# Optimization experiments

Hardware: AMD Instinct MI355X
Metric: run time of the kernel (lower is better)

Reference implementation:

```python
import jax, jax.numpy as jnp
import numpy as np
import math

EPS = 1e-5
GROUPS = 8


def setup_inputs() -> dict:
    key = jax.random.key(0)
    ks = jax.random.split(key, 4)
    B, C, H, W = 16, 256, 32, 32
    x = jax.random.normal(ks[0], (B, C, H, W), dtype=jnp.float32)
    gamma = jnp.ones((C,), dtype=jnp.float32)
    beta = jnp.zeros((C,), dtype=jnp.float32)
    # 1x1 convs are per-pixel matmuls; store weights as [out, in]
    w_qkv = jax.random.normal(ks[1], (3 * C, C), dtype=jnp.float32) * (1.0 / math.sqrt(C))
    b_qkv = jnp.zeros((3 * C,), dtype=jnp.float32)
    w_proj = jax.random.normal(ks[2], (C, C), dtype=jnp.float32) * (1.0 / math.sqrt(C))
    b_proj = jnp.zeros((C,), dtype=jnp.float32)
    return {"x": x, "gamma": gamma, "beta": beta, "w_qkv": w_qkv,
            "b_qkv": b_qkv, "w_proj": w_proj, "b_proj": b_proj}


def group_norm(x, gamma, beta):
    B, C, H, W = x.shape
    xg = x.reshape(B, GROUPS, (C // GROUPS) * H * W)
    mean = jnp.mean(xg, axis=-1, keepdims=True)
    var = jnp.var(xg, axis=-1, keepdims=True)
    xn = ((xg - mean) * jax.lax.rsqrt(var + EPS)).reshape(B, C, H, W)
    return xn * gamma[None, :, None, None] + beta[None, :, None, None]


def reference(x, gamma, beta, w_qkv, b_qkv, w_proj, b_proj):
    B, C, H, W = x.shape
    N = H * W
    residual = x
    xn = group_norm(x, gamma, beta)
    # 1x1 conv QKV: [B,3C,H,W]
    qkv = jnp.einsum('bchw,oc->bohw', xn, w_qkv) + b_qkv[None, :, None, None]
    q, k, v = jnp.split(qkv, 3, axis=1)
    q = q.reshape(B, C, N).transpose(0, 2, 1)   # [B,N,C]
    k = k.reshape(B, C, N)                      # [B,C,N]
    v = v.reshape(B, C, N).transpose(0, 2, 1)   # [B,N,C]
    attn = jnp.einsum('bnc,bcm->bnm', q, k) / math.sqrt(C)
    attn = jax.nn.softmax(attn, axis=-1)
    out = jnp.einsum('bnm,bmc->bnc', attn, v)   # [B,N,C]
    out = out.transpose(0, 2, 1).reshape(B, C, H, W)
    out = jnp.einsum('bchw,oc->bohw', out, w_proj) + b_proj[None, :, None, None]
    return out + residual
```

## Files before the change

kernel.cpp:

```cpp
#include <hip/hip_runtime.h>

typedef __bf16 bf16_t;
typedef __bf16 bf16x8 __attribute__((ext_vector_type(8)));
typedef float f32x4 __attribute__((ext_vector_type(4)));
typedef unsigned short u16;
typedef unsigned int u32;

#define MFMA16(a, b, c) __builtin_amdgcn_mfma_f32_16x16x32_bf16((a), (b), (c), 0, 0, 0)

__device__ __forceinline__ void gld_lds16(const bf16_t* g, bf16_t* l) {
  __builtin_amdgcn_global_load_lds(
      (const __attribute__((address_space(1))) void*)g,
      (__attribute__((address_space(3))) void*)l, 16, 0, 0);
}

__device__ inline bool is_f32_flag(const void* gamma) {
  return *(const u32*)gamma == 0x3F800000u;
}

template <typename T>
__device__ inline void load8f(const T* p, float* d) {
  if constexpr (sizeof(T) == 2) {
    bf16x8 v = *(const bf16x8*)p;
#pragma unroll
    for (int j = 0; j < 8; ++j) d[j] = (float)v[j];
  } else {
    float4 a = *(const float4*)p;
    float4 b = *(const float4*)(p + 4);
    d[0] = a.x; d[1] = a.y; d[2] = a.z; d[3] = a.w;
    d[4] = b.x; d[5] = b.y; d[6] = b.z; d[7] = b.w;
  }
}

__device__ inline void store8bf(bf16_t* dst, const float* s) {
  bf16x8 v;
#pragma unroll
  for (int j = 0; j < 8; ++j) v[j] = (bf16_t)s[j];
  *(bf16x8*)dst = v;
}

template <typename T>
__device__ void gn_body(const T* __restrict__ x, const T* __restrict__ gamma,
                        const T* __restrict__ beta, bf16_t* __restrict__ xn_t,
                        float* red, float* gm, float* bt) {
  const int g = blockIdx.x, b = blockIdx.y, tid = threadIdx.x;
  const T* xg = x + ((size_t)b * 256 + g * 32) * 1024;
  float sum = 0.f, sq = 0.f, v8[8];
  for (int i = tid * 8; i < 32768; i += 2048) {
    load8f(xg + i, v8);
#pragma unroll
    for (int j = 0; j < 8; ++j) { sum += v8[j]; sq += v8[j] * v8[j]; }
  }
#pragma unroll
  for (int off = 32; off; off >>= 1) {
    sum += __shfl_xor(sum, off);
    sq  += __shfl_xor(sq, off);
  }
  const int w = tid >> 6;
  if ((tid & 63) == 0) { red[w * 2] = sum; red[w * 2 + 1] = sq; }
  __syncthreads();
  sum = red[0] + red[2] + red[4] + red[6];
  sq  = red[1] + red[3] + red[5] + red[7];
  const float mean = sum * (1.f / 32768.f);
  const float var  = sq * (1.f / 32768.f) - mean * mean;
  const float rstd = rsqrtf(var + 1e-5f);
  if (tid < 32) {
    gm[tid] = (float)gamma[g * 32 + tid] * rstd;
    bt[tid] = (float)beta[g * 32 + tid];
  }
  __syncthreads();
  for (int q = 0; q < 4; ++q) {
    const int n = q * 256 + tid;
    bf16_t* dst = xn_t + ((size_t)b * 1024 + n) * 256 + g * 32;
#pragma unroll
    for (int c8 = 0; c8 < 4; ++c8) {
      bf16x8 o;
#pragma unroll
      for (int j = 0; j < 8; ++j) {
        const int c = c8 * 8 + j;
        o[j] = (bf16_t)(((float)xg[(size_t)c * 1024 + n] - mean) * gm[c] + bt[c]);
      }
      *(bf16x8*)(dst + c8 * 8) = o;
    }
  }
}

__global__ __launch_bounds__(256) void gn_kernel(const void* x, const void* gamma,
                                                 const void* beta, bf16_t* xn_t) {
  __shared__ float red[8];
  __shared__ float gm[32], bt[32];
  if (is_f32_flag(gamma))
    gn_body<float>((const float*)x, (const float*)gamma, (const float*)beta, xn_t, red, gm, bt);
  else
    gn_body<bf16_t>((const bf16_t*)x, (const bf16_t*)gamma, (const bf16_t*)beta, xn_t, red, gm, bt);
}

template <int MODE, typename T>
__device__ void gemm_body(const T* __restrict__ A, const bf16_t* __restrict__ Bt,
                          const T* __restrict__ bias, const T* __restrict__ xres,
                          void* O0v, bf16_t* __restrict__ O1, bf16_t* __restrict__ O2,
                          bf16_t* sA, bf16_t* sB) {
  const int tid = threadIdx.x;
  const int n0 = blockIdx.x * 128, m0 = blockIdx.y * 128, b = blockIdx.z;
  const bf16_t* Bb = Bt + (size_t)b * (1024 * 256);
  const int w = tid >> 6, lane = tid & 63, ln = lane & 15, quad = lane >> 4;
  const int wm = w >> 1, wn = w & 1;
  f32x4 acc[4][4] = {};
  const int sr = tid >> 3, sc = (tid & 7) * 8;
  for (int kb = 0; kb < 4; ++kb) {
    const int k0 = kb * 64;
    float t[8];
#pragma unroll 4
    for (int rr = sr; rr < 128; rr += 32) {
      load8f(A + (size_t)(m0 + rr) * 256 + k0 + sc, t);
      store8bf(sA + rr * 72 + sc, t);
      *(uint4*)(sB + rr * 72 + sc) = *(const uint4*)(Bb + (size_t)(n0 + rr) * 256 + k0 + sc);
    }
    __syncthreads();
#pragma unroll
    for (int ks = 0; ks < 2; ++ks) {
      bf16x8 af[4], bfr[4];
#pragma unroll
      for (int mt = 0; mt < 4; ++mt)
        af[mt] = *(const bf16x8*)(sA + (wm * 64 + mt * 16 + ln) * 72 + ks * 32 + quad * 8);
#pragma unroll
      for (int nt = 0; nt < 4; ++nt)
        bfr[nt] = *(const bf16x8*)(sB + (wn * 64 + nt * 16 + ln) * 72 + ks * 32 + quad * 8);
#pragma unroll
      for (int mt = 0; mt < 4; ++mt)
#pragma unroll
        for (int nt = 0; nt < 4; ++nt)
          acc[mt][nt] = MFMA16(af[mt], bfr[nt], acc[mt][nt]);
    }
    __syncthreads();
  }
  if (MODE == 0) {
    if (m0 < 512) {
      const float scale = (m0 < 256) ? 0.0625f * 1.44269504f : 1.0f;
      bf16_t* dstBase = ((m0 < 256) ? (bf16_t*)O0v : O1) + (size_t)b * (1024 * 256);
      const int osub = (m0 < 256) ? 0 : 256;
#pragma unroll
      for (int mt = 0; mt < 4; ++mt) {
        const int ob = m0 + wm * 64 + mt * 16 + quad * 4;
        float bi[4];
#pragma unroll
        for (int r = 0; r < 4; ++r) bi[r] = (float)bias[ob + r];
#pragma unroll
        for (int nt = 0; nt < 4; ++nt) {
          const int n = n0 + wn * 64 + nt * 16 + ln;
          ushort4 pk;
#pragma unroll
          for (int r = 0; r < 4; ++r) {
            bf16_t h = (bf16_t)((acc[mt][nt][r] + bi[r]) * scale);
            ((u16*)&pk)[r] = __builtin_bit_cast(u16, h);
          }
          *(ushort4*)(dstBase + (size_t)n * 256 + (ob - osub)) = pk;
        }
      }
    } else {
      bf16_t* dstV = O2 + (size_t)b * (256 * 1024);
#pragma unroll
      for (int mt = 0; mt < 4; ++mt) {
        const int ob = m0 + wm * 64 + mt * 16 + quad * 4;
        float bi[4];
#pragma unroll
        for (int r = 0; r < 4; ++r) bi[r] = (float)bias[ob + r];
#pragma unroll
        for (int nt = 0; nt < 4; ++nt) {
          const int n = n0 + wn * 64 + nt * 16 + ln;
#pragma unroll
          for (int r = 0; r < 4; ++r)
            dstV[(size_t)(ob + r - 512) * 1024 + n] = (bf16_t)(acc[mt][nt][r] + bi[r]);
        }
      }
    }
  } else {
    T* O0 = (T*)O0v;
#pragma unroll
    for (int mt = 0; mt < 4; ++mt) {
      const int ob = m0 + wm * 64 + mt * 16 + quad * 4;
      float bi[4];
#pragma unroll
      for (int r = 0; r < 4; ++r) bi[r] = (float)bias[ob + r];
#pragma unroll
      for (int nt = 0; nt < 4; ++nt) {
        const int n = n0 + wn * 64 + nt * 16 + ln;
#pragma unroll
        for (int r = 0; r < 4; ++r) {
          const size_t idx = ((size_t)b * 256 + ob + r) * 1024 + n;
          O0[idx] = (T)(acc[mt][nt][r] + bi[r] + (float)xres[idx]);
        }
      }
    }
  }
}

template <int MODE>
__global__ __launch_bounds__(256) void gemm_bt_kernel(
    const void* gflag, const void* A, const bf16_t* Bt, const void* bias,
    const void* xres, void* O0, bf16_t* O1, bf16_t* O2) {
  __shared__ alignas(16) bf16_t sA[128 * 72];
  __shared__ alignas(16) bf16_t sB[128 * 72];
  if (is_f32_flag(gflag))
    gemm_body<MODE, float>((const float*)A, Bt, (const float*)bias,
                           (const float*)xres, O0, O1, O2, sA, sB);
  else
    gemm_body<MODE, bf16_t>((const bf16_t*)A, Bt, (const bf16_t*)bias,
                            (const bf16_t*)xres, O0, O1, O2, sA, sB);
}

__global__ __launch_bounds__(256, 2) void flash_kernel(const bf16_t* __restrict__ Qt,
                                                       const bf16_t* __restrict__ Kt,
                                                       const bf16_t* __restrict__ Vc,
                                                       bf16_t* __restrict__ Ot) {
  __shared__ alignas(16) char smem[70656];
  bf16_t* sK = (bf16_t*)smem;
  bf16_t* sV = (bf16_t*)(smem + 32768);
  bf16_t* sP = (bf16_t*)(smem + 65536);
  const int bx = blockIdx.x;
  const int b = bx & 15, qt = bx >> 4;
  const int tid = threadIdx.x, w = tid >> 6, lane = tid & 63;
  const int ln = lane & 15, quad = lane >> 4;
  const int p = w >> 1, u = w & 1;
  const bf16_t* Qb = Qt + (size_t)b * 262144;
  const bf16_t* Kb = Kt + (size_t)b * 262144;
  const bf16_t* Vb = Vc + (size_t)b * 262144;
  bf16_t* sKp = sK + p * (32 * 256);
  bf16_t* sVp = sV + p * (256 * 32);
  bf16_t* sPw = sP + w * (16 * 40);

  const int hi = lane >> 5, jl = lane & 31;
  const int cvr = lane >> 2, jv = lane & 3;
  int koff[8], voff[8];
#pragma unroll
  for (int t = 0; t < 8; ++t) {
    const int m = 16 * u + 2 * t + hi;
    koff[t] = m * 256 + (jl ^ (m & 7)) * 8;
    const int c = (u * 8 + t) * 16 + cvr;
    voff[t] = c * 1024 + (jv ^ (cvr & 3)) * 8;
  }

  bf16x8 aq[8];
  {
    const bf16_t* qr = Qb + (size_t)(qt * 32 + u * 16 + ln) * 256 + quad * 8;
#pragma unroll
    for (int ks = 0; ks < 8; ++ks) aq[ks] = *(const bf16x8*)(qr + ks * 32);
  }
  bf16x8 ones;
#pragma unroll
  for (int j = 0; j < 8; ++j) ones[j] = (bf16_t)1.0f;
  f32x4 accO[16] = {};
  f32x4 lacc = {};

  for (int s = 0; s < 16; ++s) {
    const int kv0 = p * 512 + s * 32;
    const bf16_t* Ks = Kb + (size_t)kv0 * 256;
    const bf16_t* Vs = Vb + kv0;
#pragma unroll
    for (int t = 0; t < 8; ++t) {
      gld_lds16(Ks + koff[t], sKp + (u * 8 + t) * 512);
      gld_lds16(Vs + voff[t], sVp + (u * 8 + t) * 512);
    }
    __syncthreads();
    f32x4 s0 = {}, s1 = {};
#pragma unroll
    for (int ks = 0; ks < 8; ++ks) {
      const int j0 = ((ks * 4 + quad) ^ (ln & 7)) * 8;
      bf16x8 b0 = *(const bf16x8*)(sKp + ln * 256 + j0);
      bf16x8 b1 = *(const bf16x8*)(sKp + (16 + ln) * 256 + j0);
      s0 = MFMA16(aq[ks], b0, s0);
      s1 = MFMA16(aq[ks], b1, s1);
    }
#pragma unroll
    for (int r = 0; r < 4; ++r) {
      sPw[(quad * 4 + r) * 40 + ln]      = (bf16_t)exp2f(s0[r]);
      sPw[(quad * 4 + r) * 40 + 16 + ln] = (bf16_t)exp2f(s1[r]);
    }
    bf16x8 ap = *(const bf16x8*)(sPw + ln * 40 + quad * 8);
    lacc = MFMA16(ap, ones, lacc);
#pragma unroll
    for (int ct = 0; ct < 16; ++ct) {
      const int c = ct * 16 + ln;
      bf16x8 bv = *(const bf16x8*)(sVp + c * 32 + (quad ^ (ln & 3)) * 8);
      accO[ct] = MFMA16(ap, bv, accO[ct]);
    }
    __syncthreads();
  }
  f32x4* mb = (f32x4*)smem;
  if (p == 1) {
#pragma unroll
    for (int ct = 0; ct < 16; ++ct) mb[(u * 16 + ct) * 64 + lane] = accO[ct];
    mb[2048 + u * 64 + lane] = lacc;
  }
  __syncthreads();
  if (p == 0) {
    f32x4 lo = mb[2048 + u * 64 + lane];
    float linv[4];
#pragma unroll
    for (int r = 0; r < 4; ++r) linv[r] = 1.f / (lacc[r] + lo[r]);
    bf16_t* Ob = Ot + (size_t)b * 262144 + (size_t)(qt * 32 + u * 16 + quad * 4) * 256;
#pragma unroll
    for (int ct = 0; ct < 16; ++ct) {
      f32x4 o2 = mb[(u * 16 + ct) * 64 + lane];
#pragma unroll
      for (int r = 0; r < 4; ++r)
        Ob[(size_t)r * 256 + ct * 16 + ln] = (bf16_t)((accO[ct][r] + o2[r]) * linv[r]);
    }
  }
}

extern "C" void kernel_launch(void* const* d_in, const int* in_sizes, int n_in,
                              void* d_out, int out_size, void* d_ws, size_t ws_size,
                              hipStream_t stream) {
  const void* x      = d_in[0];
  const void* gamma  = d_in[1];
  const void* beta   = d_in[2];
  const void* w_qkv  = d_in[3];
  const void* b_qkv  = d_in[4];
  const void* w_proj = d_in[5];
  const void* b_proj = d_in[6];

  bf16_t* xn_t = (bf16_t*)d_ws;
  bf16_t* Qt   = xn_t + 4194304;
  bf16_t* Kt   = Qt + 4194304;
  bf16_t* Vc   = Kt + 4194304;
  bf16_t* Ot   = xn_t;

  gn_kernel<<<dim3(8, 16), 256, 0, stream>>>(x, gamma, beta, xn_t);
  gemm_bt_kernel<0><<<dim3(8, 6, 16), 256, 0, stream>>>(gamma, w_qkv, xn_t, b_qkv,
                                                        nullptr, Qt, Kt, Vc);
  flash_kernel<<<dim3(512), 256, 0, stream>>>(Qt, Kt, Vc, Ot);
  gemm_bt_kernel<1><<<dim3(8, 2, 16), 256, 0, stream>>>(gamma, w_proj, Ot, b_proj,
                                                        x, d_out, nullptr, nullptr);
}
```

Baseline: 178.9 us.

## Double flash query tile per block and load GEMM B tile via direct-to-LDS swizzle

The flash attention kernel now processes 64 query rows per block, two 16-row groups per wave, instead of 32, and is launched with 256 blocks instead of 512. Each K/V tile loaded into LDS is therefore reused by twice as many queries, halving K/V traffic per query. The cost is double the accumulator registers and dropping the launch bounds occupancy hint, so only 256 blocks run and occupancy falls. Separately, the GEMM B operand is now loaded with global_load_lds into an XOR-swizzled unpadded LDS layout instead of going through registers.

```diff
diff --git a/kernel.cpp b/kernel.cpp
--- a/kernel.cpp
+++ b/kernel.cpp
@@ -107,14 +107,20 @@
   const int wm = w >> 1, wn = w & 1;
   f32x4 acc[4][4] = {};
   const int sr = tid >> 3, sc = (tid & 7) * 8;
+  const int brl = lane >> 3;
+  const int bco = ((lane & 7) ^ brl) * 8;
   for (int kb = 0; kb < 4; ++kb) {
     const int k0 = kb * 64;
-    float t[8];
-#pragma unroll 4
+#pragma unroll
+    for (int t = 0; t < 4; ++t) {
+      const int rb = w * 32 + t * 8;
+      gld_lds16(Bb + (size_t)(n0 + rb + brl) * 256 + k0 + bco, sB + rb * 64);
+    }
+    float tt[8];
+#pragma unroll
     for (int rr = sr; rr < 128; rr += 32) {
-      load8f(A + (size_t)(m0 + rr) * 256 + k0 + sc, t);
-      store8bf(sA + rr * 72 + sc, t);
-      *(uint4*)(sB + rr * 72 + sc) = *(const uint4*)(Bb + (size_t)(n0 + rr) * 256 + k0 + sc);
+      load8f(A + (size_t)(m0 + rr) * 256 + k0 + sc, tt);
+      store8bf(sA + rr * 72 + sc, tt);
     }
     __syncthreads();
 #pragma unroll
@@ -124,8 +130,11 @@
       for (int mt = 0; mt < 4; ++mt)
         af[mt] = *(const bf16x8*)(sA + (wm * 64 + mt * 16 + ln) * 72 + ks * 32 + quad * 8);
 #pragma unroll
-      for (int nt = 0; nt < 4; ++nt)
-        bfr[nt] = *(const bf16x8*)(sB + (wn * 64 + nt * 16 + ln) * 72 + ks * 32 + quad * 8);
+      for (int nt = 0; nt < 4; ++nt) {
+        const int row = wn * 64 + nt * 16 + ln;
+        const int p = ((ks * 4 + quad) ^ (ln & 7)) * 8;
+        bfr[nt] = *(const bf16x8*)(sB + row * 64 + p);
+      }
 #pragma unroll
       for (int mt = 0; mt < 4; ++mt)
 #pragma unroll
@@ -200,7 +209,7 @@
     const void* gflag, const void* A, const bf16_t* Bt, const void* bias,
     const void* xres, void* O0, bf16_t* O1, bf16_t* O2) {
   __shared__ alignas(16) bf16_t sA[128 * 72];
-  __shared__ alignas(16) bf16_t sB[128 * 72];
+  __shared__ alignas(16) bf16_t sB[128 * 64];
   if (is_f32_flag(gflag))
     gemm_body<MODE, float>((const float*)A, Bt, (const float*)bias,
                            (const float*)xres, O0, O1, O2, sA, sB);
@@ -209,11 +218,11 @@
                             (const bf16_t*)xres, O0, O1, O2, sA, sB);
 }
 
-__global__ __launch_bounds__(256, 2) void flash_kernel(const bf16_t* __restrict__ Qt,
-                                                       const bf16_t* __restrict__ Kt,
-                                                       const bf16_t* __restrict__ Vc,
-                                                       bf16_t* __restrict__ Ot) {
-  __shared__ alignas(16) char smem[70656];
+__global__ void flash_kernel(const bf16_t* __restrict__ Qt,
+                             const bf16_t* __restrict__ Kt,
+                             const bf16_t* __restrict__ Vc,
+                             bf16_t* __restrict__ Ot) {
+  __shared__ alignas(16) char smem[75776];
   bf16_t* sK = (bf16_t*)smem;
   bf16_t* sV = (bf16_t*)(smem + 32768);
   bf16_t* sP = (bf16_t*)(smem + 65536);
@@ -227,7 +236,7 @@
   const bf16_t* Vb = Vc + (size_t)b * 262144;
   bf16_t* sKp = sK + p * (32 * 256);
   bf16_t* sVp = sV + p * (256 * 32);
-  bf16_t* sPw = sP + w * (16 * 40);
+  bf16_t* sPw = sP + w * (32 * 40);
 
   const int hi = lane >> 5, jl = lane & 31;
   const int cvr = lane >> 2, jv = lane & 3;
@@ -240,17 +249,18 @@
     voff[t] = c * 1024 + (jv ^ (cvr & 3)) * 8;
   }
 
-  bf16x8 aq[8];
-  {
-    const bf16_t* qr = Qb + (size_t)(qt * 32 + u * 16 + ln) * 256 + quad * 8;
-#pragma unroll
-    for (int ks = 0; ks < 8; ++ks) aq[ks] = *(const bf16x8*)(qr + ks * 32);
+  bf16x8 aq[2][8];
+#pragma unroll
+  for (int g = 0; g < 2; ++g) {
+    const bf16_t* qr = Qb + (size_t)(qt * 64 + u * 32 + g * 16 + ln) * 256 + quad * 8;
+#pragma unroll
+    for (int ks = 0; ks < 8; ++ks) aq[g][ks] = *(const bf16x8*)(qr + ks * 32);
   }
   bf16x8 ones;
 #pragma unroll
   for (int j = 0; j < 8; ++j) ones[j] = (bf16_t)1.0f;
-  f32x4 accO[16] = {};
-  f32x4 lacc = {};
+  f32x4 accO[2][16] = {};
+  f32x4 lacc[2] = {};
 
   for (int s = 0; s < 16; ++s) {
     const int kv0 = p * 512 + s * 32;
@@ -262,49 +272,63 @@
       gld_lds16(Vs + voff[t], sVp + (u * 8 + t) * 512);
     }
     __syncthreads();
-    f32x4 s0 = {}, s1 = {};
-#pragma unroll
-    for (int ks = 0; ks < 8; ++ks) {
-      const int j0 = ((ks * 4 + quad) ^ (ln & 7)) * 8;
-      bf16x8 b0 = *(const bf16x8*)(sKp + ln * 256 + j0);
-      bf16x8 b1 = *(const bf16x8*)(sKp + (16 + ln) * 256 + j0);
-      s0 = MFMA16(aq[ks], b0, s0);
-      s1 = MFMA16(aq[ks], b1, s1);
-    }
-#pragma unroll
-    for (int r = 0; r < 4; ++r) {
-      sPw[(quad * 4 + r) * 40 + ln]      = (bf16_t)exp2f(s0[r]);
-      sPw[(quad * 4 + r) * 40 + 16 + ln] = (bf16_t)exp2f(s1[r]);
-    }
-    bf16x8 ap = *(const bf16x8*)(sPw + ln * 40 + quad * 8);
-    lacc = MFMA16(ap, ones, lacc);
+#pragma unroll
+    for (int g = 0; g < 2; ++g) {
+      f32x4 s0 = {}, s1 = {};
+#pragma unroll
+      for (int ks = 0; ks < 8; ++ks) {
+        const int j0 = ((ks * 4 + quad) ^ (ln & 7)) * 8;
+        bf16x8 b0 = *(const bf16x8*)(sKp + ln * 256 + j0);
+        bf16x8 b1 = *(const bf16x8*)(sKp + (16 + ln) * 256 + j0);
+        s0 = MFMA16(aq[g][ks], b0, s0);
+        s1 = MFMA16(aq[g][ks], b1, s1);
+      }
+#pragma unroll
+      for (int r = 0; r < 4; ++r) {
+        sPw[(g * 16 + quad * 4 + r) * 40 + ln]      = (bf16_t)exp2f(s0[r]);
+        sPw[(g * 16 + quad * 4 + r) * 40 + 16 + ln] = (bf16_t)exp2f(s1[r]);
+      }
+    }
+    bf16x8 ap0 = *(const bf16x8*)(sPw + ln * 40 + quad * 8);
+    bf16x8 ap1 = *(const bf16x8*)(sPw + (16 + ln) * 40 + quad * 8);
+    lacc[0] = MFMA16(ap0, ones, lacc[0]);
+    lacc[1] = MFMA16(ap1, ones, lacc[1]);
 #pragma unroll
     for (int ct = 0; ct < 16; ++ct) {
       const int c = ct * 16 + ln;
       bf16x8 bv = *(const bf16x8*)(sVp + c * 32 + (quad ^ (ln & 3)) * 8);
-      accO[ct] = MFMA16(ap, bv, accO[ct]);
+      accO[0][ct] = MFMA16(ap0, bv, accO[0][ct]);
+      accO[1][ct] = MFMA16(ap1, bv, accO[1][ct]);
     }
     __syncthreads();
   }
   f32x4* mb = (f32x4*)smem;
   if (p == 1) {
 #pragma unroll
-    for (int ct = 0; ct < 16; ++ct) mb[(u * 16 + ct) * 64 + lane] = accO[ct];
-    mb[2048 + u * 64 + lane] = lacc;
+    for (int g = 0; g < 2; ++g) {
+#pragma unroll
+      for (int ct = 0; ct < 16; ++ct)
+        mb[((u * 2 + g) * 16 + ct) * 64 + lane] = accO[g][ct];
+      mb[4096 + (u * 2 + g) * 64 + lane] = lacc[g];
+    }
   }
   __syncthreads();
   if (p == 0) {
-    f32x4 lo = mb[2048 + u * 64 + lane];
-    float linv[4];
-#pragma unroll
-    for (int r = 0; r < 4; ++r) linv[r] = 1.f / (lacc[r] + lo[r]);
-    bf16_t* Ob = Ot + (size_t)b * 262144 + (size_t)(qt * 32 + u * 16 + quad * 4) * 256;
-#pragma unroll
-    for (int ct = 0; ct < 16; ++ct) {
-      f32x4 o2 = mb[(u * 16 + ct) * 64 + lane];
-#pragma unroll
-      for (int r = 0; r < 4; ++r)
-        Ob[(size_t)r * 256 + ct * 16 + ln] = (bf16_t)((accO[ct][r] + o2[r]) * linv[r]);
+#pragma unroll
+    for (int g = 0; g < 2; ++g) {
+      f32x4 lo = mb[4096 + (u * 2 + g) * 64 + lane];
+      float linv[4];
+#pragma unroll
+      for (int r = 0; r < 4; ++r) linv[r] = 1.f / (lacc[g][r] + lo[r]);
+      bf16_t* Ob = Ot + (size_t)b * 262144 +
+                   (size_t)(qt * 64 + u * 32 + g * 16 + quad * 4) * 256;
+#pragma unroll
+      for (int ct = 0; ct < 16; ++ct) {
+        f32x4 o2 = mb[((u * 2 + g) * 16 + ct) * 64 + lane];
+#pragma unroll
+        for (int r = 0; r < 4; ++r)
+          Ob[(size_t)r * 256 + ct * 16 + ln] = (bf16_t)((accO[g][ct][r] + o2[r]) * linv[r]);
+      }
     }
   }
 }
@@ -329,7 +353,7 @@
   gn_kernel<<<dim3(8, 16), 256, 0, stream>>>(x, gamma, beta, xn_t);
   gemm_bt_kernel<0><<<dim3(8, 6, 16), 256, 0, stream>>>(gamma, w_qkv, xn_t, b_qkv,
                                                         nullptr, Qt, Kt, Vc);
-  flash_kernel<<<dim3(512), 256, 0, stream>>>(Qt, Kt, Vc, Ot);
+  flash_kernel<<<dim3(256), 256, 0, stream>>>(Qt, Kt, Vc, Ot);
   gemm_bt_kernel<1><<<dim3(8, 2, 16), 256, 0, stream>>>(gamma, w_proj, Ot, b_proj,
                                                         x, d_out, nullptr, nullptr);
 }
```

Measured after the change: 318.8 us. 78.2% more time.
